# Performance work log

Measured on AMD Instinct MI355X. Metric: run time of the kernel, lower is better.

## Reference

```python
import jax, jax.numpy as jnp
import numpy as np

B, D_IN, D_HID, D_OUT = 32768, 512, 1024, 2048

def setup_inputs() -> dict:
    key = jax.random.key(0)
    k1, k2, k3, k4 = jax.random.split(key, 4)
    x = jax.random.normal(k1, (B, D_IN), dtype=jnp.float32)
    # linear1 params (torch Linear default-style init, scale approximated)
    l1_w = jax.random.normal(k2, (D_HID, D_IN), dtype=jnp.float32) * (D_IN ** -0.5)
    l1_b = jax.random.normal(k3, (D_HID,), dtype=jnp.float32) * 0.01
    # second linear params: normal(0, hidden^-0.5) weight, zero bias as in source
    weight = jax.random.normal(k4, (D_OUT, D_HID), dtype=jnp.float32) * (D_HID ** -0.5)
    bias = jnp.zeros((D_OUT,), dtype=jnp.float32)
    return {"x": x, "l1_w": l1_w, "l1_b": l1_b, "weight": weight, "bias": bias}

def reference(x, l1_w, l1_b, weight, bias):
    # linear1: [B, D_IN] -> [B, D_HID]
    h = jnp.einsum('bi,hi->bh', x, l1_w) + l1_b
    # fused linear + max epilogue: scores [B, D_OUT] -> max over output dim
    scores = jnp.einsum('bh,oh->bo', h, weight) + bias
    return jnp.max(scores, axis=-1)  # [B]
```

## Files before the change

kernel.cpp:

```cpp
#include <hip/hip_runtime.h>
#include <hip/hip_bf16.h>
#include <stdint.h>

static constexpr int BATCH = 32768;
static constexpr int DIN   = 512;
static constexpr int DHID  = 1024;
static constexpr int DOUT  = 2048;

typedef __bf16 bf16x8 __attribute__((ext_vector_type(8)));
typedef float  f32x4  __attribute__((ext_vector_type(4)));

__device__ __forceinline__ unsigned short f2bf(float f) {
    unsigned int u = __float_as_uint(f);
    u += 0x7FFFu + ((u >> 16) & 1u);
    return (unsigned short)(u >> 16);
}

__device__ __forceinline__ void gload_lds16(const void* g, void* l) {
    __builtin_amdgcn_global_load_lds((__attribute__((address_space(1))) void*)g,
                                     (__attribute__((address_space(3))) void*)l,
                                     16, 0, 0);
}


__global__ __launch_bounds__(256) void prep_kernel(
    const float* __restrict__ w1, const float4* __restrict__ w2f,
    const float4* __restrict__ xf, const float* __restrict__ b1,
    const float* __restrict__ b2,
    unsigned short* __restrict__ w1t, ushort4* __restrict__ w2b,
    ushort4* __restrict__ xb, float* __restrict__ bp) {
    const int blk = blockIdx.x;
    const int t   = threadIdx.x;
    if (blk < 512) {
        __shared__ float tile[32][33];
        const int tileI = blk & 15;
        const int tileH = blk >> 4;
        const int iBase = tileI * 32, hBase = tileH * 32;
        const int col = t & 31, rowq = t >> 5;
#pragma unroll
        for (int p = 0; p < 4; ++p) {
            const int row = p * 8 + rowq;
            tile[row][col] = w1[(size_t)(hBase + row) * DIN + iBase + col];
        }
        __syncthreads();
#pragma unroll
        for (int p = 0; p < 4; ++p) {
            const int row = p * 8 + rowq;
            w1t[(size_t)(iBase + row) * DHID + hBase + col] = f2bf(tile[col][row]);
        }
    } else if (blk < 2560) {
        __shared__ float wsum[4];
        const int o = blk - 512;
        const size_t g = (size_t)o * 256 + t;
        float4 v = w2f[g];
        ushort4 ob;
        ob.x = f2bf(v.x); ob.y = f2bf(v.y); ob.z = f2bf(v.z); ob.w = f2bf(v.w);
        w2b[g] = ob;
        float4 bv = ((const float4*)b1)[t];
        float s = v.x * bv.x + v.y * bv.y + v.z * bv.z + v.w * bv.w;
#pragma unroll
        for (int off = 1; off < 64; off <<= 1) s += __shfl_xor(s, off);
        if ((t & 63) == 0) wsum[t >> 6] = s;
        __syncthreads();
        if (t == 0) bp[o] = wsum[0] + wsum[1] + wsum[2] + wsum[3] + b2[o];
    } else {
        const size_t g = (size_t)(blk - 2560) * 256 + t;
        float4 v = xf[g];
        ushort4 o;
        o.x = f2bf(v.x); o.y = f2bf(v.y); o.z = f2bf(v.z); o.w = f2bf(v.w);
        xb[g] = o;
    }
}

__global__ __launch_bounds__(256) void gemmW_kernel(
    const unsigned short* __restrict__ A,
    const unsigned short* __restrict__ Bw,
    unsigned short* __restrict__ W) {
    constexpr int K = DHID;
    __shared__ __align__(16) unsigned short sA[64 * 128];
    __shared__ __align__(16) unsigned short sB[64 * 128];

    const int tid  = threadIdx.x;
    const int lane = tid & 63;
    const int wid  = tid >> 6;
    const int wr = wid >> 1, wc = wid & 1;
    const int r = lane & 15, q = lane >> 4;
    const int blockN = blockIdx.x * 64;
    const int blockM = blockIdx.y * 64;

    const int chKey = (tid & 15) ^ ((tid >> 4) & 15);
    const size_t aBase = (size_t)(blockM + (tid >> 4)) * K + chKey * 8;
    const size_t bBase = (size_t)(blockN + (tid >> 4)) * K + chKey * 8;

    f32x4 acc[2][2];
#pragma unroll
    for (int mt = 0; mt < 2; ++mt)
#pragma unroll
        for (int nt = 0; nt < 2; ++nt) { f32x4 z = {0.f, 0.f, 0.f, 0.f}; acc[mt][nt] = z; }

    for (int k0 = 0; k0 < K; k0 += 128) {
#pragma unroll
        for (int j = 0; j < 4; ++j) {
            gload_lds16(A  + aBase + (size_t)j * 16 * K + k0, sA + j * 2048 + wid * 512);
            gload_lds16(Bw + bBase + (size_t)j * 16 * K + k0, sB + j * 2048 + wid * 512);
        }
        __syncthreads();
#pragma unroll
        for (int ks = 0; ks < 4; ++ks) {
            const int ch = ((ks << 2) + q) ^ r;
            bf16x8 af[2], bf[2];
#pragma unroll
            for (int mt = 0; mt < 2; ++mt) af[mt] = *(const bf16x8*)&sA[(wr * 32 + mt * 16 + r) * 128 + ch * 8];
#pragma unroll
            for (int nt = 0; nt < 2; ++nt) bf[nt] = *(const bf16x8*)&sB[(wc * 32 + nt * 16 + r) * 128 + ch * 8];
#pragma unroll
            for (int mt = 0; mt < 2; ++mt)
#pragma unroll
                for (int nt = 0; nt < 2; ++nt)
                    acc[mt][nt] = __builtin_amdgcn_mfma_f32_16x16x32_bf16(af[mt], bf[nt], acc[mt][nt], 0, 0, 0);
        }
        __syncthreads();
    }

#pragma unroll
    for (int mt = 0; mt < 2; ++mt) {
        const int row0 = blockM + wr * 32 + mt * 16 + q * 4;
#pragma unroll
        for (int nt = 0; nt < 2; ++nt) {
            const int col = blockN + wc * 32 + nt * 16 + r;
#pragma unroll
            for (int reg = 0; reg < 4; ++reg)
                W[(size_t)(row0 + reg) * DIN + col] = f2bf(acc[mt][nt][reg]);
        }
    }
}

__global__ __launch_bounds__(512, 2) void gemmS_kernel(
    const unsigned short* __restrict__ A,
    const unsigned short* __restrict__ Bw,
    const float* __restrict__ bp,
    float* __restrict__ partials) {
    constexpr int K = DIN;
    __shared__ __align__(16) unsigned short lds[51200];

    const int tid  = threadIdx.x;
    const int lane = tid & 63;
    const int wid  = tid >> 6;
    const int wr   = wid >> 1;
    const int wc   = wid & 1;
    const int r    = lane & 15, q = lane >> 4;

    const int b     = blockIdx.x;
    const int xcd   = b & 7;
    const int j     = b >> 3;
    const int nHalf = j & 1;
    const int blockM = (xcd * 16 + (j >> 1)) * 256;
    const int nBase  = nHalf * 1024;

    const int sRow = tid >> 2;
    const int swz  = (tid & 3) ^ ((tid >> 3) & 3);
    const unsigned short* aSrc = A  + (size_t)(blockM + sRow) * K + swz * 8;
    const unsigned short* bCur = Bw + (size_t)(nBase  + sRow) * K + swz * 8;
    float* biasLds = (float*)(lds + 49152);

#define STAGE_A(ptr, buf, kh, kt) do {                                          \
    gload_lds16((ptr) + (kt) * 64 + (kh) * 32,                                  \
                lds + (buf) * 16384 + (kh) * 8192 + wid * 512);                 \
    gload_lds16((ptr) + 128 * K + (kt) * 64 + (kh) * 32,                        \
                lds + (buf) * 16384 + (kh) * 8192 + 4096 + wid * 512);          \
} while (0)
#define STAGE_B(ptr, buf, kh, kt) do {                                          \
    gload_lds16((ptr) + (kt) * 64 + (kh) * 32,                                  \
                lds + 32768 + (buf) * 8192 + (kh) * 4096 + wid * 512);          \
} while (0)

    const int rsw  = (r >> 1) & 3;
    const int fOff = (q ^ rsw) * 8;
    const unsigned short* ldsAf = lds + (wr * 64 + r) * 32 + fOff;
    const unsigned short* ldsBf = lds + 32768 + (wc * 64 + r) * 32 + fOff;

    f32x4 acc[4][4];
#pragma unroll
    for (int mt = 0; mt < 4; ++mt)
#pragma unroll
        for (int nt = 0; nt < 4; ++nt) { f32x4 z = {0.f, 0.f, 0.f, 0.f}; acc[mt][nt] = z; }
    float mx[4][4];
#pragma unroll
    for (int mt = 0; mt < 4; ++mt)
#pragma unroll
        for (int rg = 0; rg < 4; ++rg) mx[mt][rg] = -INFINITY;
    bf16x8 af[4], bfr[4];
    float bvc[4];

#define LDA(buf, kh) do {                                                       \
    const unsigned short* p_ = ldsAf + (buf) * 16384 + (kh) * 8192;             \
    af[0] = *(const bf16x8*)(p_);                                               \
    af[1] = *(const bf16x8*)(p_ + 512);                                         \
    af[2] = *(const bf16x8*)(p_ + 1024);                                        \
    af[3] = *(const bf16x8*)(p_ + 1536);                                        \
} while (0)
#define LDB(buf, kh) do {                                                       \
    const unsigned short* p_ = ldsBf + (buf) * 8192 + (kh) * 4096;              \
    bfr[0] = *(const bf16x8*)(p_);                                              \
    bfr[1] = *(const bf16x8*)(p_ + 512);                                        \
    bfr[2] = *(const bf16x8*)(p_ + 1024);                                       \
    bfr[3] = *(const bf16x8*)(p_ + 1536);                                       \
} while (0)
#define MM() do {                                                               \
    __builtin_amdgcn_s_setprio(1);                                              \
    _Pragma("unroll") for (int m_ = 0; m_ < 4; ++m_)                            \
    _Pragma("unroll") for (int n_ = 0; n_ < 4; ++n_)                            \
        acc[m_][n_] = __builtin_amdgcn_mfma_f32_16x16x32_bf16(                  \
            af[m_], bfr[n_], acc[m_][n_], 0, 0, 0);                             \
    __builtin_amdgcn_s_setprio(0);                                              \
} while (0)
#define BAR()   __builtin_amdgcn_s_barrier()
#define LGKM0() asm volatile("s_waitcnt lgkmcnt(0)" ::: "memory")
#define VMC(n)  asm volatile("s_waitcnt vmcnt(" #n ")" ::: "memory")

#define FOLD() do {                                                             \
    _Pragma("unroll") for (int mt_ = 0; mt_ < 4; ++mt_)                         \
    _Pragma("unroll") for (int rg_ = 0; rg_ < 4; ++rg_) {                       \
        float v_ = fmaxf(fmaxf(acc[mt_][0][rg_] + bvc[0],                       \
                               acc[mt_][1][rg_] + bvc[1]),                      \
                         fmaxf(acc[mt_][2][rg_] + bvc[2],                       \
                               acc[mt_][3][rg_] + bvc[3]));                     \
        mx[mt_][rg_] = fmaxf(mx[mt_][rg_], v_);                                 \
    }                                                                           \
} while (0)
#define ACC_ZERO() do {                                                         \
    _Pragma("unroll") for (int mt_ = 0; mt_ < 4; ++mt_)                         \
    _Pragma("unroll") for (int nt_ = 0; nt_ < 4; ++nt_) {                       \
        f32x4 z_ = {0.f, 0.f, 0.f, 0.f}; acc[mt_][nt_] = z_;                    \
    }                                                                           \
} while (0)

    {
        float2 bb = ((const float2*)(bp + nBase))[tid];
        ((float2*)biasLds)[tid] = bb;
    }
    LGKM0();

    STAGE_A(aSrc, 0, 0, 0); STAGE_B(bCur, 0, 0, 0);
    STAGE_A(aSrc, 0, 1, 0); STAGE_B(bCur, 0, 1, 0);
    STAGE_A(aSrc, 1, 0, 1); STAGE_B(bCur, 1, 0, 1);
    VMC(3);
    BAR();

#pragma unroll
    for (int nt = 0; nt < 4; ++nt) bvc[nt] = biasLds[wc * 64 + nt * 16 + r];

#pragma unroll 1
    for (int ntile = 0; ntile < 8; ++ntile) {
#pragma unroll 1
        for (int it = 0; it < 3; ++it) {
            const int k1 = 2 * it + 1, k2 = 2 * it + 2, k3 = 2 * it + 3;
            LDA(0, 0); LDB(0, 0);
            STAGE_A(aSrc, 1, 1, k1); STAGE_B(bCur, 1, 1, k1); VMC(6);
            LGKM0(); MM(); BAR();
            LDA(0, 1); LDB(0, 1);
            STAGE_A(aSrc, 0, 0, k2); STAGE_B(bCur, 0, 0, k2); VMC(6);
            LGKM0(); MM(); BAR();
            LDA(1, 0); LDB(1, 0);
            STAGE_A(aSrc, 0, 1, k2); STAGE_B(bCur, 0, 1, k2); VMC(6);
            LGKM0(); MM(); BAR();
            LDA(1, 1); LDB(1, 1);
            STAGE_A(aSrc, 1, 0, k3); STAGE_B(bCur, 1, 0, k3); VMC(6);
            LGKM0(); MM(); BAR();
        }
        if (ntile < 7) {
            const unsigned short* bNxt = bCur + 128 * K;
            LDA(0, 0); LDB(0, 0);
            STAGE_A(aSrc, 1, 1, 7); STAGE_B(bCur, 1, 1, 7); VMC(6);
            LGKM0(); MM(); BAR();
            LDA(0, 1); LDB(0, 1);
            STAGE_A(aSrc, 0, 0, 0); STAGE_B(bNxt, 0, 0, 0); VMC(6);
            LGKM0(); MM(); BAR();
            LDA(1, 0); LDB(1, 0);
            STAGE_A(aSrc, 0, 1, 0); STAGE_B(bNxt, 0, 1, 0); VMC(6);
            LGKM0(); MM(); BAR();
            LDA(1, 1); LDB(1, 1);
            STAGE_A(aSrc, 1, 0, 1); STAGE_B(bNxt, 1, 0, 1); VMC(6);
            LGKM0(); MM(); BAR();
            FOLD();
            ACC_ZERO();
#pragma unroll
            for (int nt = 0; nt < 4; ++nt)
                bvc[nt] = biasLds[(ntile + 1) * 128 + wc * 64 + nt * 16 + r];
            bCur = bNxt;
        } else {
            LDA(0, 0); LDB(0, 0);
            STAGE_A(aSrc, 1, 1, 7); STAGE_B(bCur, 1, 1, 7); VMC(6);
            LGKM0(); MM(); BAR();
            LDA(0, 1); LDB(0, 1); VMC(3);
            LGKM0(); MM(); BAR();
            LDA(1, 0); LDB(1, 0); VMC(0);
            LGKM0(); MM(); BAR();
            LDA(1, 1); LDB(1, 1);
            LGKM0(); MM();
            FOLD();
        }
    }

#undef STAGE_A
#undef STAGE_B
#undef LDA
#undef LDB
#undef MM
#undef BAR
#undef LGKM0
#undef VMC
#undef FOLD
#undef ACC_ZERO

#pragma unroll
    for (int mt = 0; mt < 4; ++mt) {
#pragma unroll
        for (int rg = 0; rg < 4; ++rg) {
            float v = mx[mt][rg];
#pragma unroll
            for (int off = 1; off < 16; off <<= 1)
                v = fmaxf(v, __shfl_xor(v, off));
            if (r == 0) {
                const int row = blockM + wr * 64 + mt * 16 + q * 4 + rg;
                partials[(size_t)row * 4 + nHalf * 2 + wc] = v;
            }
        }
    }
}

__global__ __launch_bounds__(256) void reduce_kernel(
    const float4* __restrict__ partials, float* __restrict__ out) {
    const int row = blockIdx.x * blockDim.x + threadIdx.x;
    float4 v = partials[row];
    out[row] = fmaxf(fmaxf(v.x, v.y), fmaxf(v.z, v.w));
}

extern "C" void kernel_launch(void* const* d_in, const int* in_sizes, int n_in,
                              void* d_out, int out_size, void* d_ws, size_t ws_size,
                              hipStream_t stream) {
    const float* x   = (const float*)d_in[0];
    const float* l1w = (const float*)d_in[1];
    const float* l1b = (const float*)d_in[2];
    const float* w2  = (const float*)d_in[3];
    const float* b2  = (const float*)d_in[4];
    float* out = (float*)d_out;

    char* ws = (char*)d_ws;
    unsigned short* w1t = (unsigned short*)(ws);
    unsigned short* w2b = (unsigned short*)(ws + 1048576);
    unsigned short* Wb  = (unsigned short*)(ws + 5242880);
    float* bp           = (float*)(ws + 7340032);
    unsigned short* xb  = (unsigned short*)(ws + 7348224);
    float* partials     = (float*)(ws + 40902656);

    prep_kernel<<<18944, 256, 0, stream>>>(
        l1w, (const float4*)w2, (const float4*)x, l1b, b2,
        w1t, (ushort4*)w2b, (ushort4*)xb, bp);

    gemmW_kernel<<<dim3(DIN / 64, DOUT / 64), 256, 0, stream>>>(w2b, w1t, Wb);

    gemmS_kernel<<<256, 512, 0, stream>>>(xb, Wb, bp, partials);

    reduce_kernel<<<BATCH / 256, 256, 0, stream>>>((const float4*)partials, out);
}
```

Baseline: 183.2 us.

## Double-buffer MFMA fragments to overlap LDS reads with compute in fused GEMM

Restructures the gemmS main loop so LDS fragment reads for the next phase (into alternating even/odd register sets) are issued before the MFMAs of the current phase, so LDS latency overlaps with matrix math instead of waiting on lgkmcnt before each MFMA block. The loop is unrolled by n-tile with sched_barrier fences after each barrier to keep the compiler from reordering phases. The prep kernel's x-conversion path also handles four float4s per thread, cutting the grid from 18944 to 6656 blocks. The cost is doubled fragment registers, which may pressure occupancy, and a much longer unrolled code body.

After: 191.3 us. 1.04x slower.

```diff
diff --git a/kernel.cpp b/kernel.cpp
--- a/kernel.cpp
+++ b/kernel.cpp
@@ -64,11 +64,14 @@
         __syncthreads();
         if (t == 0) bp[o] = wsum[0] + wsum[1] + wsum[2] + wsum[3] + b2[o];
     } else {
-        const size_t g = (size_t)(blk - 2560) * 256 + t;
-        float4 v = xf[g];
-        ushort4 o;
-        o.x = f2bf(v.x); o.y = f2bf(v.y); o.z = f2bf(v.z); o.w = f2bf(v.w);
-        xb[g] = o;
+        const size_t base = (size_t)(blk - 2560) * 1024 + t;
+#pragma unroll
+        for (int i = 0; i < 4; ++i) {
+            float4 v = xf[base + i * 256];
+            ushort4 o;
+            o.x = f2bf(v.x); o.y = f2bf(v.y); o.z = f2bf(v.z); o.w = f2bf(v.w);
+            xb[base + i * 256] = o;
+        }
     }
 }
 
@@ -189,32 +192,51 @@
     for (int mt = 0; mt < 4; ++mt)
 #pragma unroll
         for (int rg = 0; rg < 4; ++rg) mx[mt][rg] = -INFINITY;
-    bf16x8 af[4], bfr[4];
+    bf16x8 afE[4], bfrE[4], afO[4], bfrO[4];
     float bvc[4];
 
-#define LDA(buf, kh) do {                                                       \
-    const unsigned short* p_ = ldsAf + (buf) * 16384 + (kh) * 8192;             \
-    af[0] = *(const bf16x8*)(p_);                                               \
-    af[1] = *(const bf16x8*)(p_ + 512);                                         \
-    af[2] = *(const bf16x8*)(p_ + 1024);                                        \
-    af[3] = *(const bf16x8*)(p_ + 1536);                                        \
-} while (0)
-#define LDB(buf, kh) do {                                                       \
-    const unsigned short* p_ = ldsBf + (buf) * 8192 + (kh) * 4096;              \
-    bfr[0] = *(const bf16x8*)(p_);                                              \
-    bfr[1] = *(const bf16x8*)(p_ + 512);                                        \
-    bfr[2] = *(const bf16x8*)(p_ + 1024);                                       \
-    bfr[3] = *(const bf16x8*)(p_ + 1536);                                       \
-} while (0)
-#define MM() do {                                                               \
+#define RD_E(rb, rk) do {                                                       \
+    const unsigned short* pa_ = ldsAf + (rb) * 16384 + (rk) * 8192;             \
+    afE[0] = *(const bf16x8*)(pa_);                                             \
+    afE[1] = *(const bf16x8*)(pa_ + 512);                                       \
+    afE[2] = *(const bf16x8*)(pa_ + 1024);                                      \
+    afE[3] = *(const bf16x8*)(pa_ + 1536);                                      \
+    const unsigned short* pb_ = ldsBf + (rb) * 8192 + (rk) * 4096;              \
+    bfrE[0] = *(const bf16x8*)(pb_);                                            \
+    bfrE[1] = *(const bf16x8*)(pb_ + 512);                                      \
+    bfrE[2] = *(const bf16x8*)(pb_ + 1024);                                     \
+    bfrE[3] = *(const bf16x8*)(pb_ + 1536);                                     \
+} while (0)
+#define RD_O(rb, rk) do {                                                       \
+    const unsigned short* pa_ = ldsAf + (rb) * 16384 + (rk) * 8192;             \
+    afO[0] = *(const bf16x8*)(pa_);                                             \
+    afO[1] = *(const bf16x8*)(pa_ + 512);                                       \
+    afO[2] = *(const bf16x8*)(pa_ + 1024);                                      \
+    afO[3] = *(const bf16x8*)(pa_ + 1536);                                      \
+    const unsigned short* pb_ = ldsBf + (rb) * 8192 + (rk) * 4096;              \
+    bfrO[0] = *(const bf16x8*)(pb_);                                            \
+    bfrO[1] = *(const bf16x8*)(pb_ + 512);                                      \
+    bfrO[2] = *(const bf16x8*)(pb_ + 1024);                                     \
+    bfrO[3] = *(const bf16x8*)(pb_ + 1536);                                     \
+} while (0)
+#define MM_E() do {                                                             \
     __builtin_amdgcn_s_setprio(1);                                              \
     _Pragma("unroll") for (int m_ = 0; m_ < 4; ++m_)                            \
     _Pragma("unroll") for (int n_ = 0; n_ < 4; ++n_)                            \
         acc[m_][n_] = __builtin_amdgcn_mfma_f32_16x16x32_bf16(                  \
-            af[m_], bfr[n_], acc[m_][n_], 0, 0, 0);                             \
+            afE[m_], bfrE[n_], acc[m_][n_], 0, 0, 0);                           \
     __builtin_amdgcn_s_setprio(0);                                              \
 } while (0)
-#define BAR()   __builtin_amdgcn_s_barrier()
+#define MM_O() do {                                                             \
+    __builtin_amdgcn_s_setprio(1);                                              \
+    _Pragma("unroll") for (int m_ = 0; m_ < 4; ++m_)                            \
+    _Pragma("unroll") for (int n_ = 0; n_ < 4; ++n_)                            \
+        acc[m_][n_] = __builtin_amdgcn_mfma_f32_16x16x32_bf16(                  \
+            afO[m_], bfrO[n_], acc[m_][n_], 0, 0, 0);                           \
+    __builtin_amdgcn_s_setprio(0);                                              \
+} while (0)
+#define BARS()  do { __builtin_amdgcn_s_barrier();                              \
+                     __builtin_amdgcn_sched_barrier(0); } while (0)
 #define LGKM0() asm volatile("s_waitcnt lgkmcnt(0)" ::: "memory")
 #define VMC(n)  asm volatile("s_waitcnt vmcnt(" #n ")" ::: "memory")
 
@@ -235,6 +257,32 @@
     }                                                                           \
 } while (0)
 
+#define PH(RS, rb, rk, MS, BP, sb, sk, st)  do {                                \
+    RD_##RS(rb, rk);                                                            \
+    STAGE_A(aSrc, sb, sk, st); STAGE_B(BP, sb, sk, st);                         \
+    MM_##MS();                                                                  \
+    VMC(6); LGKM0(); BARS();                                                    \
+} while (0)
+
+#define PHASES_1_12(BP)                                                         \
+    PH(O, 0, 1, E, BP, 0, 0, 2);                                                \
+    PH(E, 1, 0, O, BP, 0, 1, 2);                                                \
+    PH(O, 1, 1, E, BP, 1, 0, 3);                                                \
+    PH(E, 0, 0, O, BP, 1, 1, 3);                                                \
+    PH(O, 0, 1, E, BP, 0, 0, 4);                                                \
+    PH(E, 1, 0, O, BP, 0, 1, 4);                                                \
+    PH(O, 1, 1, E, BP, 1, 0, 5);                                                \
+    PH(E, 0, 0, O, BP, 1, 1, 5);                                                \
+    PH(O, 0, 1, E, BP, 0, 0, 6);                                                \
+    PH(E, 1, 0, O, BP, 0, 1, 6);                                                \
+    PH(O, 1, 1, E, BP, 1, 0, 7);                                                \
+    PH(E, 0, 0, O, BP, 1, 1, 7);
+
+#define PHASES_13_15(BPN)                                                       \
+    PH(O, 0, 1, E, BPN, 0, 0, 0);                                               \
+    PH(E, 1, 0, O, BPN, 0, 1, 0);                                               \
+    PH(O, 1, 1, E, BPN, 1, 0, 1);
+
     {
         float2 bb = ((const float2*)(bp + nBase))[tid];
         ((float2*)biasLds)[tid] = bb;
@@ -245,73 +293,66 @@
     STAGE_A(aSrc, 0, 1, 0); STAGE_B(bCur, 0, 1, 0);
     STAGE_A(aSrc, 1, 0, 1); STAGE_B(bCur, 1, 0, 1);
     VMC(3);
-    BAR();
+    BARS();
 
 #pragma unroll
     for (int nt = 0; nt < 4; ++nt) bvc[nt] = biasLds[wc * 64 + nt * 16 + r];
 
+    RD_E(0, 0);
+    STAGE_A(aSrc, 1, 1, 1); STAGE_B(bCur, 1, 1, 1);
+    VMC(6); LGKM0(); BARS();
+    PHASES_1_12(bCur);
+    {
+        const unsigned short* bNxt = bCur + 128 * K;
+        PHASES_13_15(bNxt);
+        bCur = bNxt;
+    }
+
+    int bOff = 128;
 #pragma unroll 1
-    for (int ntile = 0; ntile < 8; ++ntile) {
-#pragma unroll 1
-        for (int it = 0; it < 3; ++it) {
-            const int k1 = 2 * it + 1, k2 = 2 * it + 2, k3 = 2 * it + 3;
-            LDA(0, 0); LDB(0, 0);
-            STAGE_A(aSrc, 1, 1, k1); STAGE_B(bCur, 1, 1, k1); VMC(6);
-            LGKM0(); MM(); BAR();
-            LDA(0, 1); LDB(0, 1);
-            STAGE_A(aSrc, 0, 0, k2); STAGE_B(bCur, 0, 0, k2); VMC(6);
-            LGKM0(); MM(); BAR();
-            LDA(1, 0); LDB(1, 0);
-            STAGE_A(aSrc, 0, 1, k2); STAGE_B(bCur, 0, 1, k2); VMC(6);
-            LGKM0(); MM(); BAR();
-            LDA(1, 1); LDB(1, 1);
-            STAGE_A(aSrc, 1, 0, k3); STAGE_B(bCur, 1, 0, k3); VMC(6);
-            LGKM0(); MM(); BAR();
-        }
-        if (ntile < 7) {
-            const unsigned short* bNxt = bCur + 128 * K;
-            LDA(0, 0); LDB(0, 0);
-            STAGE_A(aSrc, 1, 1, 7); STAGE_B(bCur, 1, 1, 7); VMC(6);
-            LGKM0(); MM(); BAR();
-            LDA(0, 1); LDB(0, 1);
-            STAGE_A(aSrc, 0, 0, 0); STAGE_B(bNxt, 0, 0, 0); VMC(6);
-            LGKM0(); MM(); BAR();
-            LDA(1, 0); LDB(1, 0);
-            STAGE_A(aSrc, 0, 1, 0); STAGE_B(bNxt, 0, 1, 0); VMC(6);
-            LGKM0(); MM(); BAR();
-            LDA(1, 1); LDB(1, 1);
-            STAGE_A(aSrc, 1, 0, 1); STAGE_B(bNxt, 1, 0, 1); VMC(6);
-            LGKM0(); MM(); BAR();
-            FOLD();
-            ACC_ZERO();
-#pragma unroll
-            for (int nt = 0; nt < 4; ++nt)
-                bvc[nt] = biasLds[(ntile + 1) * 128 + wc * 64 + nt * 16 + r];
-            bCur = bNxt;
-        } else {
-            LDA(0, 0); LDB(0, 0);
-            STAGE_A(aSrc, 1, 1, 7); STAGE_B(bCur, 1, 1, 7); VMC(6);
-            LGKM0(); MM(); BAR();
-            LDA(0, 1); LDB(0, 1); VMC(3);
-            LGKM0(); MM(); BAR();
-            LDA(1, 0); LDB(1, 0); VMC(0);
-            LGKM0(); MM(); BAR();
-            LDA(1, 1); LDB(1, 1);
-            LGKM0(); MM();
-            FOLD();
-        }
-    }
+    for (int t = 1; t < 7; ++t) {
+        RD_E(0, 0);
+        STAGE_A(aSrc, 1, 1, 1); STAGE_B(bCur, 1, 1, 1);
+        MM_O();
+        FOLD(); ACC_ZERO();
+#pragma unroll
+        for (int nt = 0; nt < 4; ++nt) bvc[nt] = biasLds[bOff + wc * 64 + nt * 16 + r];
+        VMC(6); LGKM0(); BARS();
+        PHASES_1_12(bCur);
+        const unsigned short* bNxt = bCur + 128 * K;
+        PHASES_13_15(bNxt);
+        bCur = bNxt;
+        bOff += 128;
+    }
+
+    RD_E(0, 0);
+    STAGE_A(aSrc, 1, 1, 1); STAGE_B(bCur, 1, 1, 1);
+    MM_O();
+    FOLD(); ACC_ZERO();
+#pragma unroll
+    for (int nt = 0; nt < 4; ++nt) bvc[nt] = biasLds[896 + wc * 64 + nt * 16 + r];
+    VMC(6); LGKM0(); BARS();
+    PHASES_1_12(bCur);
+    RD_O(0, 1); MM_E(); VMC(3); LGKM0(); BARS();
+    RD_E(1, 0); MM_O(); VMC(0); LGKM0(); BARS();
+    RD_O(1, 1); MM_E(); LGKM0();
+    MM_O();
+    FOLD();
 
 #undef STAGE_A
 #undef STAGE_B
-#undef LDA
-#undef LDB
-#undef MM
-#undef BAR
+#undef RD_E
+#undef RD_O
+#undef MM_E
+#undef MM_O
+#undef BARS
 #undef LGKM0
 #undef VMC
 #undef FOLD
 #undef ACC_ZERO
+#undef PH
+#undef PHASES_1_12
+#undef PHASES_13_15
 
 #pragma unroll
     for (int mt = 0; mt < 4; ++mt) {
@@ -354,7 +395,7 @@
     unsigned short* xb  = (unsigned short*)(ws + 7348224);
     float* partials     = (float*)(ws + 40902656);
 
-    prep_kernel<<<18944, 256, 0, stream>>>(
+    prep_kernel<<<6656, 256, 0, stream>>>(
         l1w, (const float4*)w2, (const float4*)x, l1b, b2,
         w1t, (ushort4*)w2b, (ushort4*)xb, bp);
 
```

## Retile score GEMM to 64-row blocks over full N, drop reduce kernel

Applied to the files above, without the earlier changes.

The main score GEMM now uses 256-thread blocks that each own 64 batch rows and sweep all 2048 outputs in 256-column tiles. A 4-deep LDS ring buffer with 32-wide K steps replaces the previous double buffer. Because each block covers the full output dimension, the row max is finished in LDS and written straight to the output, so the partials buffer and the separate reduce kernel go away. The x-to-bf16 conversion in the prep kernel also handles four float4s per thread with fewer blocks. In exchange, A tiles are smaller, so each loaded B tile is reused across fewer rows, and there are more barriers per K step.

Result: slower. 203.0 us (+10.8%).

```diff
diff --git a/kernel.cpp b/kernel.cpp
--- a/kernel.cpp
+++ b/kernel.cpp
@@ -64,11 +64,14 @@
         __syncthreads();
         if (t == 0) bp[o] = wsum[0] + wsum[1] + wsum[2] + wsum[3] + b2[o];
     } else {
-        const size_t g = (size_t)(blk - 2560) * 256 + t;
-        float4 v = xf[g];
-        ushort4 o;
-        o.x = f2bf(v.x); o.y = f2bf(v.y); o.z = f2bf(v.z); o.w = f2bf(v.w);
-        xb[g] = o;
+        const size_t base = (size_t)(blk - 2560) * 1024 + t;
+#pragma unroll
+        for (int i = 0; i < 4; ++i) {
+            float4 v = xf[base + i * 256];
+            ushort4 o;
+            o.x = f2bf(v.x); o.y = f2bf(v.y); o.z = f2bf(v.z); o.w = f2bf(v.w);
+            xb[base + i * 256] = o;
+        }
     }
 }
 
@@ -135,49 +138,45 @@
     }
 }
 
-__global__ __launch_bounds__(512, 2) void gemmS_kernel(
+__global__ __launch_bounds__(256, 2) void gemmS_kernel(
     const unsigned short* __restrict__ A,
     const unsigned short* __restrict__ Bw,
     const float* __restrict__ bp,
-    float* __restrict__ partials) {
+    float* __restrict__ out) {
     constexpr int K = DIN;
-    __shared__ __align__(16) unsigned short lds[51200];
+    __shared__ __align__(16) unsigned short lds[40960];
 
     const int tid  = threadIdx.x;
     const int lane = tid & 63;
     const int wid  = tid >> 6;
-    const int wr   = wid >> 1;
-    const int wc   = wid & 1;
     const int r    = lane & 15, q = lane >> 4;
 
-    const int b     = blockIdx.x;
-    const int xcd   = b & 7;
-    const int j     = b >> 3;
-    const int nHalf = j & 1;
-    const int blockM = (xcd * 16 + (j >> 1)) * 256;
-    const int nBase  = nHalf * 1024;
+    const int b    = blockIdx.x;
+    const int xcd  = b & 7;
+    const int j    = b >> 3;
+    const int blockM = (xcd * 64 + j) * 64;
 
     const int sRow = tid >> 2;
     const int swz  = (tid & 3) ^ ((tid >> 3) & 3);
     const unsigned short* aSrc = A  + (size_t)(blockM + sRow) * K + swz * 8;
-    const unsigned short* bCur = Bw + (size_t)(nBase  + sRow) * K + swz * 8;
-    float* biasLds = (float*)(lds + 49152);
-
-#define STAGE_A(ptr, buf, kh, kt) do {                                          \
-    gload_lds16((ptr) + (kt) * 64 + (kh) * 32,                                  \
-                lds + (buf) * 16384 + (kh) * 8192 + wid * 512);                 \
-    gload_lds16((ptr) + 128 * K + (kt) * 64 + (kh) * 32,                        \
-                lds + (buf) * 16384 + (kh) * 8192 + 4096 + wid * 512);          \
-} while (0)
-#define STAGE_B(ptr, buf, kh, kt) do {                                          \
-    gload_lds16((ptr) + (kt) * 64 + (kh) * 32,                                  \
-                lds + 32768 + (buf) * 8192 + (kh) * 4096 + wid * 512);          \
-} while (0)
-
-    const int rsw  = (r >> 1) & 3;
-    const int fOff = (q ^ rsw) * 8;
-    const unsigned short* ldsAf = lds + (wr * 64 + r) * 32 + fOff;
-    const unsigned short* ldsBf = lds + 32768 + (wc * 64 + r) * 32 + fOff;
+    const unsigned short* bSrc = Bw + (size_t)sRow * K + swz * 8;
+
+#define STAGE_A(reg, kt) \
+    gload_lds16(aSrc + (kt) * 32, lds + (reg) * 2048 + wid * 512)
+#define STAGE_B(bT, reg, kt) do {                                               \
+    gload_lds16((bT) + (size_t)(0 * 64) * K + (kt) * 32,                        \
+                lds + 8192 + (reg) * 8192 + 0 * 2048 + wid * 512);              \
+    gload_lds16((bT) + (size_t)(1 * 64) * K + (kt) * 32,                        \
+                lds + 8192 + (reg) * 8192 + 1 * 2048 + wid * 512);              \
+    gload_lds16((bT) + (size_t)(2 * 64) * K + (kt) * 32,                        \
+                lds + 8192 + (reg) * 8192 + 2 * 2048 + wid * 512);              \
+    gload_lds16((bT) + (size_t)(3 * 64) * K + (kt) * 32,                        \
+                lds + 8192 + (reg) * 8192 + 3 * 2048 + wid * 512);              \
+} while (0)
+
+    const int fOff = (q ^ ((r >> 1) & 3)) * 8;
+    const unsigned short* ldsAf = lds + r * 32 + fOff;
+    const unsigned short* ldsBf = lds + 8192 + (wid * 64 + r) * 32 + fOff;
 
     f32x4 acc[4][4];
 #pragma unroll
@@ -190,21 +189,19 @@
 #pragma unroll
         for (int rg = 0; rg < 4; ++rg) mx[mt][rg] = -INFINITY;
     bf16x8 af[4], bfr[4];
-    float bvc[4];
-
-#define LDA(buf, kh) do {                                                       \
-    const unsigned short* p_ = ldsAf + (buf) * 16384 + (kh) * 8192;             \
-    af[0] = *(const bf16x8*)(p_);                                               \
-    af[1] = *(const bf16x8*)(p_ + 512);                                         \
-    af[2] = *(const bf16x8*)(p_ + 1024);                                        \
-    af[3] = *(const bf16x8*)(p_ + 1536);                                        \
-} while (0)
-#define LDB(buf, kh) do {                                                       \
-    const unsigned short* p_ = ldsBf + (buf) * 8192 + (kh) * 4096;              \
-    bfr[0] = *(const bf16x8*)(p_);                                              \
-    bfr[1] = *(const bf16x8*)(p_ + 512);                                        \
-    bfr[2] = *(const bf16x8*)(p_ + 1024);                                       \
-    bfr[3] = *(const bf16x8*)(p_ + 1536);                                       \
+    float bvc[4], bvn[4];
+
+#define RD(reg) do {                                                            \
+    const unsigned short* pa_ = ldsAf + (reg) * 2048;                           \
+    af[0] = *(const bf16x8*)(pa_);                                              \
+    af[1] = *(const bf16x8*)(pa_ + 512);                                        \
+    af[2] = *(const bf16x8*)(pa_ + 1024);                                       \
+    af[3] = *(const bf16x8*)(pa_ + 1536);                                       \
+    const unsigned short* pb_ = ldsBf + (reg) * 8192;                           \
+    bfr[0] = *(const bf16x8*)(pb_);                                             \
+    bfr[1] = *(const bf16x8*)(pb_ + 512);                                       \
+    bfr[2] = *(const bf16x8*)(pb_ + 1024);                                      \
+    bfr[3] = *(const bf16x8*)(pb_ + 1536);                                      \
 } while (0)
 #define MM() do {                                                               \
     __builtin_amdgcn_s_setprio(1);                                              \
@@ -217,6 +214,22 @@
 #define BAR()   __builtin_amdgcn_s_barrier()
 #define LGKM0() asm volatile("s_waitcnt lgkmcnt(0)" ::: "memory")
 #define VMC(n)  asm volatile("s_waitcnt vmcnt(" #n ")" ::: "memory")
+
+#define PH(reg, sreg, skt, bT) do {                                             \
+    RD(reg);                                                                    \
+    STAGE_A(sreg, skt); STAGE_B(bT, sreg, skt);                                 \
+    VMC(10); LGKM0(); MM(); BAR();                                              \
+} while (0)
+#define PH15(reg, sreg, skt, bT, bOff) do {                                     \
+    RD(reg);                                                                    \
+    bvn[0] = bp[(bOff) + wid * 64 + 0 * 16 + r];                                \
+    bvn[1] = bp[(bOff) + wid * 64 + 1 * 16 + r];                                \
+    bvn[2] = bp[(bOff) + wid * 64 + 2 * 16 + r];                                \
+    bvn[3] = bp[(bOff) + wid * 64 + 3 * 16 + r];                                \
+    __builtin_amdgcn_sched_barrier(0);                                          \
+    STAGE_A(sreg, skt); STAGE_B(bT, sreg, skt);                                 \
+    VMC(10); LGKM0(); MM(); BAR();                                              \
+} while (0)
 
 #define FOLD() do {                                                             \
     _Pragma("unroll") for (int mt_ = 0; mt_ < 4; ++mt_)                         \
@@ -235,84 +248,76 @@
     }                                                                           \
 } while (0)
 
+#pragma unroll
+    for (int nt = 0; nt < 4; ++nt) bvc[nt] = bp[wid * 64 + nt * 16 + r];
+    VMC(0);
+
+    STAGE_A(0, 0); STAGE_B(bSrc, 0, 0);
+    STAGE_A(1, 1); STAGE_B(bSrc, 1, 1);
+    STAGE_A(2, 2); STAGE_B(bSrc, 2, 2);
+    VMC(10);
+    BAR();
+
+#pragma unroll 1
+    for (int t = 0; t < 7; ++t) {
+        const unsigned short* bT  = bSrc + (size_t)t * 256 * K;
+        const unsigned short* bTn = bT + (size_t)256 * K;
+        PH(0, 3, 3, bT);
+        PH(1, 0, 4, bT);
+        PH(2, 1, 5, bT);
+        PH(3, 2, 6, bT);
+        PH(0, 3, 7, bT);
+        PH(1, 0, 8, bT);
+        PH(2, 1, 9, bT);
+        PH(3, 2, 10, bT);
+        PH(0, 3, 11, bT);
+        PH(1, 0, 12, bT);
+        PH(2, 1, 13, bT);
+        PH(3, 2, 14, bT);
+        PH(0, 3, 15, bT);
+        PH(1, 0, 0, bTn);
+        PH(2, 1, 1, bTn);
+        PH15(3, 2, 2, bTn, (t + 1) * 256);
+        FOLD();
+        ACC_ZERO();
+#pragma unroll
+        for (int nt = 0; nt < 4; ++nt) bvc[nt] = bvn[nt];
+    }
     {
-        float2 bb = ((const float2*)(bp + nBase))[tid];
-        ((float2*)biasLds)[tid] = bb;
-    }
-    LGKM0();
-
-    STAGE_A(aSrc, 0, 0, 0); STAGE_B(bCur, 0, 0, 0);
-    STAGE_A(aSrc, 0, 1, 0); STAGE_B(bCur, 0, 1, 0);
-    STAGE_A(aSrc, 1, 0, 1); STAGE_B(bCur, 1, 0, 1);
-    VMC(3);
-    BAR();
-
-#pragma unroll
-    for (int nt = 0; nt < 4; ++nt) bvc[nt] = biasLds[wc * 64 + nt * 16 + r];
-
-#pragma unroll 1
-    for (int ntile = 0; ntile < 8; ++ntile) {
-#pragma unroll 1
-        for (int it = 0; it < 3; ++it) {
-            const int k1 = 2 * it + 1, k2 = 2 * it + 2, k3 = 2 * it + 3;
-            LDA(0, 0); LDB(0, 0);
-            STAGE_A(aSrc, 1, 1, k1); STAGE_B(bCur, 1, 1, k1); VMC(6);
-            LGKM0(); MM(); BAR();
-            LDA(0, 1); LDB(0, 1);
-            STAGE_A(aSrc, 0, 0, k2); STAGE_B(bCur, 0, 0, k2); VMC(6);
-            LGKM0(); MM(); BAR();
-            LDA(1, 0); LDB(1, 0);
-            STAGE_A(aSrc, 0, 1, k2); STAGE_B(bCur, 0, 1, k2); VMC(6);
-            LGKM0(); MM(); BAR();
-            LDA(1, 1); LDB(1, 1);
-            STAGE_A(aSrc, 1, 0, k3); STAGE_B(bCur, 1, 0, k3); VMC(6);
-            LGKM0(); MM(); BAR();
-        }
-        if (ntile < 7) {
-            const unsigned short* bNxt = bCur + 128 * K;
-            LDA(0, 0); LDB(0, 0);
-            STAGE_A(aSrc, 1, 1, 7); STAGE_B(bCur, 1, 1, 7); VMC(6);
-            LGKM0(); MM(); BAR();
-            LDA(0, 1); LDB(0, 1);
-            STAGE_A(aSrc, 0, 0, 0); STAGE_B(bNxt, 0, 0, 0); VMC(6);
-            LGKM0(); MM(); BAR();
-            LDA(1, 0); LDB(1, 0);
-            STAGE_A(aSrc, 0, 1, 0); STAGE_B(bNxt, 0, 1, 0); VMC(6);
-            LGKM0(); MM(); BAR();
-            LDA(1, 1); LDB(1, 1);
-            STAGE_A(aSrc, 1, 0, 1); STAGE_B(bNxt, 1, 0, 1); VMC(6);
-            LGKM0(); MM(); BAR();
-            FOLD();
-            ACC_ZERO();
-#pragma unroll
-            for (int nt = 0; nt < 4; ++nt)
-                bvc[nt] = biasLds[(ntile + 1) * 128 + wc * 64 + nt * 16 + r];
-            bCur = bNxt;
-        } else {
-            LDA(0, 0); LDB(0, 0);
-            STAGE_A(aSrc, 1, 1, 7); STAGE_B(bCur, 1, 1, 7); VMC(6);
-            LGKM0(); MM(); BAR();
-            LDA(0, 1); LDB(0, 1); VMC(3);
-            LGKM0(); MM(); BAR();
-            LDA(1, 0); LDB(1, 0); VMC(0);
-            LGKM0(); MM(); BAR();
-            LDA(1, 1); LDB(1, 1);
-            LGKM0(); MM();
-            FOLD();
-        }
+        const unsigned short* bT = bSrc + (size_t)7 * 256 * K;
+        PH(0, 3, 3, bT);
+        PH(1, 0, 4, bT);
+        PH(2, 1, 5, bT);
+        PH(3, 2, 6, bT);
+        PH(0, 3, 7, bT);
+        PH(1, 0, 8, bT);
+        PH(2, 1, 9, bT);
+        PH(3, 2, 10, bT);
+        PH(0, 3, 11, bT);
+        PH(1, 0, 12, bT);
+        PH(2, 1, 13, bT);
+        PH(3, 2, 14, bT);
+        PH(0, 3, 15, bT);
+        RD(1); VMC(5); LGKM0(); MM(); BAR();
+        RD(2); VMC(0); LGKM0(); MM(); BAR();
+        RD(3); LGKM0(); MM();
+        FOLD();
     }
 
 #undef STAGE_A
 #undef STAGE_B
-#undef LDA
-#undef LDB
+#undef RD
 #undef MM
 #undef BAR
 #undef LGKM0
 #undef VMC
+#undef PH
+#undef PH15
 #undef FOLD
 #undef ACC_ZERO
 
+    __syncthreads();
+    float* smax = (float*)lds;
 #pragma unroll
     for (int mt = 0; mt < 4; ++mt) {
 #pragma unroll
@@ -321,19 +326,14 @@
 #pragma unroll
             for (int off = 1; off < 16; off <<= 1)
                 v = fmaxf(v, __shfl_xor(v, off));
-            if (r == 0) {
-                const int row = blockM + wr * 64 + mt * 16 + q * 4 + rg;
-                partials[(size_t)row * 4 + nHalf * 2 + wc] = v;
-            }
-        }
-    }
-}
-
-__global__ __launch_bounds__(256) void reduce_kernel(
-    const float4* __restrict__ partials, float* __restrict__ out) {
-    const int row = blockIdx.x * blockDim.x + threadIdx.x;
-    float4 v = partials[row];
-    out[row] = fmaxf(fmaxf(v.x, v.y), fmaxf(v.z, v.w));
+            if (r == 0) smax[(mt * 16 + q * 4 + rg) * 4 + wid] = v;
+        }
+    }
+    __syncthreads();
+    if (tid < 64) {
+        const float* p = smax + tid * 4;
+        out[blockM + tid] = fmaxf(fmaxf(p[0], p[1]), fmaxf(p[2], p[3]));
+    }
 }
 
 extern "C" void kernel_launch(void* const* d_in, const int* in_sizes, int n_in,
@@ -352,15 +352,12 @@
     unsigned short* Wb  = (unsigned short*)(ws + 5242880);
     float* bp           = (float*)(ws + 7340032);
     unsigned short* xb  = (unsigned short*)(ws + 7348224);
-    float* partials     = (float*)(ws + 40902656);
-
-    prep_kernel<<<18944, 256, 0, stream>>>(
+
+    prep_kernel<<<6656, 256, 0, stream>>>(
         l1w, (const float4*)w2, (const float4*)x, l1b, b2,
         w1t, (ushort4*)w2b, (ushort4*)xb, bp);
 
     gemmW_kernel<<<dim3(DIN / 64, DOUT / 64), 256, 0, stream>>>(w2b, w1t, Wb);
 
-    gemmS_kernel<<<256, 512, 0, stream>>>(xb, Wb, bp, partials);
-
-    reduce_kernel<<<BATCH / 256, 256, 0, stream>>>((const float4*)partials, out);
-}
+    gemmS_kernel<<<512, 256, 0, stream>>>(xb, Wb, bp, out);
+}
```
